# Performance work log

Measured on AMD Instinct MI355X. Metric: run time of the kernel, lower is better.

Reference implementation:

```python
import jax, jax.numpy as jnp
import numpy as np

N_NODES = 50000
N_EDGES = 320000
IN_FEAT = 128
HIDDEN = 256
N_CLASSES = 40
BN_EPS = 1e-5


def _gcn_norm(edge_index, n_nodes):
    # Add self-loops (PyG gcn_norm default) and compute sym-normalized weights
    loops = jnp.arange(n_nodes, dtype=edge_index.dtype)
    src = jnp.concatenate([edge_index[0], loops])
    dst = jnp.concatenate([edge_index[1], loops])
    ones = jnp.ones(src.shape[0], dtype=jnp.float32)
    deg = jax.ops.segment_sum(ones, dst, num_segments=n_nodes)
    dinv = jnp.where(deg > 0, jax.lax.rsqrt(deg), 0.0)
    norm = dinv[src] * dinv[dst]  # [E+N]
    return src, dst, norm


def _gcn_conv(x, src, dst, norm, W, b, n_nodes):
    xw = x @ W                                   # [N, F_out]
    msg = norm[:, None] * xw[src]                # [E+N, F_out] gather
    out = jax.ops.segment_sum(msg, dst, num_segments=n_nodes)  # scatter-add
    return out + b


def _batchnorm(x, gamma, beta):
    mean = jnp.mean(x, axis=0)
    var = jnp.mean(jnp.square(x - mean), axis=0)  # biased, training-mode stats
    return (x - mean) * jax.lax.rsqrt(var + BN_EPS) * gamma + beta


def setup_inputs() -> dict:
    key = jax.random.key(0)
    ks = jax.random.split(key, 8)
    x = jax.random.normal(ks[0], (N_NODES, IN_FEAT), dtype=jnp.float32)
    edge_index = jax.random.randint(ks[1], (2, N_EDGES), 0, N_NODES, dtype=jnp.int64)
    s1 = 1.0 / np.sqrt(IN_FEAT)
    s2 = 1.0 / np.sqrt(HIDDEN)
    return {
        "x": x,
        "edge_index": edge_index,
        "W1": jax.random.normal(ks[2], (IN_FEAT, HIDDEN), dtype=jnp.float32) * s1,
        "b1": jnp.zeros((HIDDEN,), dtype=jnp.float32),
        "g1": jnp.ones((HIDDEN,), dtype=jnp.float32),
        "be1": jnp.zeros((HIDDEN,), dtype=jnp.float32),
        "W2": jax.random.normal(ks[3], (HIDDEN, HIDDEN), dtype=jnp.float32) * s2,
        "b2": jnp.zeros((HIDDEN,), dtype=jnp.float32),
        "g2": jnp.ones((HIDDEN,), dtype=jnp.float32),
        "be2": jnp.zeros((HIDDEN,), dtype=jnp.float32),
        "W3": jax.random.normal(ks[4], (HIDDEN, N_CLASSES), dtype=jnp.float32) * s2,
        "b3": jnp.zeros((N_CLASSES,), dtype=jnp.float32),
    }


def reference(x, edge_index, W1, b1, g1, be1, W2, b2, g2, be2, W3, b3):
    n = x.shape[0]
    src, dst, norm = _gcn_norm(edge_index, n)
    # layer 1
    h = _gcn_conv(x, src, dst, norm, W1, b1, n)
    h = jax.nn.relu(_batchnorm(h, g1, be1))
    # layer 2
    h = _gcn_conv(h, src, dst, norm, W2, b2, n)
    h = jax.nn.relu(_batchnorm(h, g2, be2))
    # output layer
    h = _gcn_conv(h, src, dst, norm, W3, b3, n)
    return jax.nn.log_softmax(h, axis=1)
```

## Files before the change

### kernel.cpp

```cpp
#include <hip/hip_runtime.h>

#define N_NODES 50000
#define N_EDGES 320000
#define IN_FEAT 128
#define HIDDEN  256
#define NCLS    40
#define BN_EPS  1e-5f

#define SCAN_B  256
#define SCAN_NB ((N_NODES + SCAN_B - 1) / SCAN_B)
#define GNB     (N_NODES / 16)

#define PREP_HIST_NB  (N_EDGES / 256)
#define PREP_CVT_NB   (N_NODES * IN_FEAT / 8 / 256)
#define PREP_PACK_NB  54
#define BNA_NB        (N_NODES * HIDDEN / 8 / 256)

typedef __attribute__((ext_vector_type(8))) _Float16 f16x8;
typedef __attribute__((ext_vector_type(2))) _Float16 f16x2;
typedef __attribute__((ext_vector_type(4))) float f32x4;

__device__ __forceinline__ f16x2 pkmax0(f16x2 a) {
    return __builtin_elementwise_max(a, (f16x2)(_Float16)0.f);
}

__device__ __forceinline__ void packB_unit(const float* __restrict__ W,
                                           _Float16* __restrict__ Bp,
                                           int nt, int kt, int nkt, int M, int lane) {
    const int n = nt * 16 + (lane & 15);
    const int kb = kt * 32 + (lane >> 4) * 8;
    _Float16* dst = Bp + (((size_t)nt * nkt + kt) * 64 + lane) * 8;
#pragma unroll
    for (int j = 0; j < 8; j++)
        dst[j] = (n < M) ? (_Float16)W[(size_t)(kb + j) * M + n] : (_Float16)0.f;
}

__global__ __launch_bounds__(256) void k_prep(const int* __restrict__ e_dst,
                                              int* __restrict__ counts,
                                              const float* __restrict__ x,
                                              _Float16* __restrict__ Xh,
                                              const float* __restrict__ W1,
                                              const float* __restrict__ W2,
                                              const float* __restrict__ W3,
                                              _Float16* __restrict__ W1p,
                                              _Float16* __restrict__ W2p,
                                              _Float16* __restrict__ W3p) {
    const int b = blockIdx.x;
    const int tid = threadIdx.x;
    if (b < PREP_HIST_NB) {
        const int e = b * 256 + tid;
        atomicAdd(&counts[e_dst[e]], 1);
    } else if (b < PREP_HIST_NB + PREP_CVT_NB) {
        const int i = (b - PREP_HIST_NB) * 256 + tid;
        float4 a = *(const float4*)(x + (size_t)i * 8);
        float4 c = *(const float4*)(x + (size_t)i * 8 + 4);
        f16x8 o = {(_Float16)a.x, (_Float16)a.y, (_Float16)a.z, (_Float16)a.w,
                   (_Float16)c.x, (_Float16)c.y, (_Float16)c.z, (_Float16)c.w};
        *(f16x8*)&Xh[(size_t)i * 8] = o;
    } else {
        const int wave = tid >> 6, lane = tid & 63;
        const int u = (b - PREP_HIST_NB - PREP_CVT_NB) * 4 + wave;
        if (u < 64) {
            packB_unit(W1, W1p, u >> 2, u & 3, 4, HIDDEN, lane);
        } else if (u < 192) {
            const int v = u - 64;
            packB_unit(W2, W2p, v >> 3, v & 7, 8, HIDDEN, lane);
        } else {
            const int v = u - 192;
            packB_unit(W3, W3p, v >> 3, v & 7, 8, NCLS, lane);
        }
    }
}

__global__ __launch_bounds__(SCAN_B) void k_scan_local(const int* __restrict__ counts,
                                                       int* __restrict__ rowp,
                                                       int* __restrict__ partials) {
    __shared__ int s[SCAN_B];
    const int tid = threadIdx.x;
    const int i = blockIdx.x * SCAN_B + tid;
    int v = (i < N_NODES) ? counts[i] : 0;
    s[tid] = v;
    __syncthreads();
    for (int off = 1; off < SCAN_B; off <<= 1) {
        int t = (tid >= off) ? s[tid - off] : 0;
        __syncthreads();
        s[tid] += t;
        __syncthreads();
    }
    if (i < N_NODES) rowp[i] = s[tid] - v;
    if (tid == SCAN_B - 1) partials[blockIdx.x] = s[SCAN_B - 1];
}

__global__ __launch_bounds__(SCAN_B) void k_scan_add(int* __restrict__ rowp,
                                                     int* __restrict__ cursor,
                                                     const int* __restrict__ partials,
                                                     const int* __restrict__ counts,
                                                     float* __restrict__ dinv) {
    __shared__ int s[SCAN_B];
    const int tid = threadIdx.x;
    const int b = blockIdx.x;
    int v = (tid < b) ? partials[tid] : 0;
    s[tid] = v;
    __syncthreads();
    for (int off = SCAN_B / 2; off > 0; off >>= 1) {
        if (tid < off) s[tid] += s[tid + off];
        __syncthreads();
    }
    const int offset = s[0];
    const int i = b * SCAN_B + tid;
    if (i < N_NODES) {
        int r = rowp[i] + offset;
        rowp[i] = r;
        cursor[i] = r;
        dinv[i] = rsqrtf(1.0f + (float)counts[i]);
    }
    if (b == 0 && tid == 0) rowp[N_NODES] = N_EDGES;
}

__global__ void k_scatter(const int* __restrict__ src, const int* __restrict__ dst,
                          int* __restrict__ cursor, const float* __restrict__ dinv,
                          int2* __restrict__ edat) {
    int e = blockIdx.x * blockDim.x + threadIdx.x;
    if (e < N_EDGES) {
        int d = dst[e], s = src[e];
        int p = atomicAdd(&cursor[d], 1);
        int2 v; v.x = s; v.y = __float_as_int(dinv[s] * dinv[d]);
        edat[p] = v;
    }
}

template <int KIN>
__global__ __launch_bounds__(256, 4) void k_fused(const _Float16* __restrict__ Xin,
                                                  const int* __restrict__ rowp,
                                                  const int2* __restrict__ edat,
                                                  const float* __restrict__ dinv,
                                                  const _Float16* __restrict__ Bp,
                                                  const float* __restrict__ bias,
                                                  _Float16* __restrict__ C,
                                                  float* __restrict__ bnp2) {
    constexpr int nkt = KIN / 32;
    constexpr int LROW = KIN + 8;
    constexpr int RW8 = KIN / 8;
    constexpr int NL = KIN / 128;
    __shared__ __align__(16) _Float16 At[16 * LROW];
    const int wave = threadIdx.x >> 6;
    const int lane = threadIdx.x & 63;
    const int sub  = lane >> 4;
    const int t    = lane & 15;
    const int sb   = lane & 48;
    const int node = blockIdx.x * 16 + wave * 4 + sub;

    const int e0 = rowp[node];
    const int deg = rowp[node + 1] - e0;
    int   pidx = 0;
    float pw   = 0.f;
    if (t < deg) {
        const int2 e = edat[e0 + t];
        pidx = e.x;
        pw = __int_as_float(e.y);
    }
    const float dd = dinv[node];
    const f16x2 sw2 = (f16x2)(_Float16)(dd * dd);

    const f16x8* __restrict__ Xr = (const f16x8*)Xin;
    union U8 { f16x8 v; f16x2 h[4]; };

    U8 a[NL];
#pragma unroll
    for (int q = 0; q < NL; q++) {
        U8 r; r.v = Xr[(size_t)node * RW8 + q * 16 + t];
#pragma unroll
        for (int p = 0; p < 4; p++) a[q].h[p] = sw2 * r.h[p];
    }

    auto fmaacc = [&](U8& r, _Float16 w, int q) {
        const f16x2 w2 = (f16x2)w;
#pragma unroll
        for (int p = 0; p < 4; p++) a[q].h[p] = w2 * r.h[p] + a[q].h[p];
    };

    if constexpr (NL == 1) {
        int bi[16]; _Float16 bw[16];
#pragma unroll
        for (int j = 0; j < 16; j++) {
            const int   v  = __shfl(pidx, sb + j);
            const float wv = __shfl(pw,  sb + j);
            const bool ok = j < deg;
            bi[j] = ok ? v : node;
            bw[j] = ok ? (_Float16)wv : (_Float16)0.f;
        }
        U8 r0, r1, r2, r3, r4, r5, r6, r7, r8, r9, r10, r11, r12, r13, r14, r15;
        r0.v  = Xr[(size_t)bi[0]  * RW8 + t];
        r1.v  = Xr[(size_t)bi[1]  * RW8 + t];
        r2.v  = Xr[(size_t)bi[2]  * RW8 + t];
        r3.v  = Xr[(size_t)bi[3]  * RW8 + t];
        r4.v  = Xr[(size_t)bi[4]  * RW8 + t];
        r5.v  = Xr[(size_t)bi[5]  * RW8 + t];
        r6.v  = Xr[(size_t)bi[6]  * RW8 + t];
        r7.v  = Xr[(size_t)bi[7]  * RW8 + t];
        r8.v  = Xr[(size_t)bi[8]  * RW8 + t];
        r9.v  = Xr[(size_t)bi[9]  * RW8 + t];
        r10.v = Xr[(size_t)bi[10] * RW8 + t];
        r11.v = Xr[(size_t)bi[11] * RW8 + t];
        r12.v = Xr[(size_t)bi[12] * RW8 + t];
        r13.v = Xr[(size_t)bi[13] * RW8 + t];
        r14.v = Xr[(size_t)bi[14] * RW8 + t];
        r15.v = Xr[(size_t)bi[15] * RW8 + t];
        asm volatile("" : "+v"(r0.v), "+v"(r1.v), "+v"(r2.v), "+v"(r3.v),
                          "+v"(r4.v), "+v"(r5.v), "+v"(r6.v), "+v"(r7.v),
                          "+v"(r8.v), "+v"(r9.v), "+v"(r10.v), "+v"(r11.v),
                          "+v"(r12.v), "+v"(r13.v), "+v"(r14.v), "+v"(r15.v));
        fmaacc(r0, bw[0], 0);   fmaacc(r1, bw[1], 0);
        fmaacc(r2, bw[2], 0);   fmaacc(r3, bw[3], 0);
        fmaacc(r4, bw[4], 0);   fmaacc(r5, bw[5], 0);
        fmaacc(r6, bw[6], 0);   fmaacc(r7, bw[7], 0);
        fmaacc(r8, bw[8], 0);   fmaacc(r9, bw[9], 0);
        fmaacc(r10, bw[10], 0); fmaacc(r11, bw[11], 0);
        fmaacc(r12, bw[12], 0); fmaacc(r13, bw[13], 0);
        fmaacc(r14, bw[14], 0); fmaacc(r15, bw[15], 0);
    } else {
        auto batch8 = [&](int j0) {
            int bi[8]; _Float16 bw[8];
#pragma unroll
            for (int j = 0; j < 8; j++) {
                const int   v  = __shfl(pidx, sb + j0 + j);
                const float wv = __shfl(pw,  sb + j0 + j);
                const bool ok = (j0 + j) < deg;
                bi[j] = ok ? v : node;
                bw[j] = ok ? (_Float16)wv : (_Float16)0.f;
            }
            U8 r0, r1, r2, r3, r4, r5, r6, r7;
            U8 s0, s1, s2, s3, s4, s5, s6, s7;
            r0.v = Xr[(size_t)bi[0] * RW8 + t];
            s0.v = Xr[(size_t)bi[0] * RW8 + 16 + t];
            r1.v = Xr[(size_t)bi[1] * RW8 + t];
            s1.v = Xr[(size_t)bi[1] * RW8 + 16 + t];
            r2.v = Xr[(size_t)bi[2] * RW8 + t];
            s2.v = Xr[(size_t)bi[2] * RW8 + 16 + t];
            r3.v = Xr[(size_t)bi[3] * RW8 + t];
            s3.v = Xr[(size_t)bi[3] * RW8 + 16 + t];
            r4.v = Xr[(size_t)bi[4] * RW8 + t];
            s4.v = Xr[(size_t)bi[4] * RW8 + 16 + t];
            r5.v = Xr[(size_t)bi[5] * RW8 + t];
            s5.v = Xr[(size_t)bi[5] * RW8 + 16 + t];
            r6.v = Xr[(size_t)bi[6] * RW8 + t];
            s6.v = Xr[(size_t)bi[6] * RW8 + 16 + t];
            r7.v = Xr[(size_t)bi[7] * RW8 + t];
            s7.v = Xr[(size_t)bi[7] * RW8 + 16 + t];
            asm volatile("" : "+v"(r0.v), "+v"(r1.v), "+v"(r2.v), "+v"(r3.v),
                              "+v"(r4.v), "+v"(r5.v), "+v"(r6.v), "+v"(r7.v),
                              "+v"(s0.v), "+v"(s1.v), "+v"(s2.v), "+v"(s3.v),
                              "+v"(s4.v), "+v"(s5.v), "+v"(s6.v), "+v"(s7.v));
            fmaacc(r0, bw[0], 0); fmaacc(s0, bw[0], 1);
            fmaacc(r1, bw[1], 0); fmaacc(s1, bw[1], 1);
            fmaacc(r2, bw[2], 0); fmaacc(s2, bw[2], 1);
            fmaacc(r3, bw[3], 0); fmaacc(s3, bw[3], 1);
            fmaacc(r4, bw[4], 0); fmaacc(s4, bw[4], 1);
            fmaacc(r5, bw[5], 0); fmaacc(s5, bw[5], 1);
            fmaacc(r6, bw[6], 0); fmaacc(s6, bw[6], 1);
            fmaacc(r7, bw[7], 0); fmaacc(s7, bw[7], 1);
        };
        batch8(0);
        if (__any(deg > 8)) batch8(8);
    }
    if (__any(deg > 16)) {
        for (int j = 16; j < deg; j++) {
            const int2 ed = edat[e0 + j];
            const f16x2 w2 = (f16x2)(_Float16)__int_as_float(ed.y);
#pragma unroll
            for (int q = 0; q < NL; q++) {
                U8 r; r.v = Xr[(size_t)ed.x * RW8 + q * 16 + t];
#pragma unroll
                for (int p = 0; p < 4; p++) a[q].h[p] = w2 * r.h[p] + a[q].h[p];
            }
        }
    }
#pragma unroll
    for (int q = 0; q < NL; q++)
        *(f16x8*)&At[(wave * 4 + sub) * LROW + q * 128 + t * 8] = a[q].v;
    __syncthreads();

    const int rowb = blockIdx.x * 16;
    const int ntile0 = wave * 4;
    const _Float16* aL = &At[(lane & 15) * LROW + (lane >> 4) * 8];
    f32x4 acc[4] = {};
#pragma unroll
    for (int kt = 0; kt < nkt; kt++) {
        f16x8 af = *(const f16x8*)(aL + kt * 32);
#pragma unroll
        for (int nt = 0; nt < 4; nt++) {
            f16x8 bfr = *(const f16x8*)(Bp + (((size_t)(ntile0 + nt) * nkt + kt) * 64 + lane) * 8);
            acc[nt] = __builtin_amdgcn_mfma_f32_16x16x32_f16(af, bfr, acc[nt], 0, 0, 0);
        }
    }
    const int rg = lane >> 4, cc = lane & 15;
    float s[4], q2[4];
#pragma unroll
    for (int nt = 0; nt < 4; nt++) {
        const int col = (ntile0 + nt) * 16 + cc;
        const float b = bias[col];
        f32x4 a2 = acc[nt];
        a2[0] += b; a2[1] += b; a2[2] += b; a2[3] += b;
        const size_t base = (size_t)(rowb + rg * 4) * HIDDEN + col;
#pragma unroll
        for (int i = 0; i < 4; i++) C[base + (size_t)i * HIDDEN] = (_Float16)a2[i];
        s[nt] = a2[0] + a2[1] + a2[2] + a2[3];
        q2[nt] = a2[0]*a2[0] + a2[1]*a2[1] + a2[2]*a2[2] + a2[3]*a2[3];
    }
#pragma unroll
    for (int nt = 0; nt < 4; nt++) {
        s[nt] += __shfl_xor(s[nt], 16); s[nt] += __shfl_xor(s[nt], 32);
        q2[nt] += __shfl_xor(q2[nt], 16); q2[nt] += __shfl_xor(q2[nt], 32);
    }
    if (lane < 16) {
        float* dst = bnp2 + ((blockIdx.x & 31) * 512) + ntile0 * 16 + lane;
#pragma unroll
        for (int nt = 0; nt < 4; nt++) {
            atomicAdd(&dst[nt * 16], s[nt]);
            atomicAdd(&dst[nt * 16 + 256], q2[nt]);
        }
    }
}

__global__ __launch_bounds__(256) void k_bnprep(const float* __restrict__ bnp2,
                                                const float* __restrict__ g,
                                                const float* __restrict__ be,
                                                float* __restrict__ scale,
                                                float* __restrict__ shift) {
    const int f = threadIdx.x;
    float s = 0.f, q = 0.f;
#pragma unroll
    for (int b = 0; b < 32; b++) {
        s += bnp2[(size_t)b * 512 + f];
        q += bnp2[(size_t)b * 512 + 256 + f];
    }
    const float inv_n = 1.0f / (float)N_NODES;
    float mean = s * inv_n;
    float var = q * inv_n - mean * mean;
    var = fmaxf(var, 0.f);
    float sc = g[f] * rsqrtf(var + BN_EPS);
    scale[f] = sc;
    shift[f] = be[f] - mean * sc;
}

__global__ __launch_bounds__(256) void k_bnapply(_Float16* __restrict__ H,
                                                 const float* __restrict__ scale,
                                                 const float* __restrict__ shift) {
    const size_t i = (size_t)blockIdx.x * 256 + threadIdx.x;
    const int f0 = (int)(i & 31) * 8;
    union U8 { f16x8 v; f16x2 h[4]; } r;
    r.v = ((const f16x8*)H)[i];
#pragma unroll
    for (int p = 0; p < 4; p++) {
        f16x2 sc = {(_Float16)scale[f0 + 2 * p], (_Float16)scale[f0 + 2 * p + 1]};
        f16x2 sh = {(_Float16)shift[f0 + 2 * p], (_Float16)shift[f0 + 2 * p + 1]};
        r.h[p] = pkmax0(sc * r.h[p] + sh);
    }
    ((f16x8*)H)[i] = r.v;
}

template <int K_>
__global__ __launch_bounds__(64) void k_gemm3(const _Float16* __restrict__ A,
                                              const _Float16* __restrict__ Bp,
                                              const float* __restrict__ scale,
                                              const float* __restrict__ shift,
                                              _Float16* __restrict__ C) {
    constexpr int nkt = K_ / 32;
    constexpr int MT = 3;
    const int lane = threadIdx.x & 63;
    const int rowb = blockIdx.x * 16;
    const int koff = (lane >> 4) * 8;
    const _Float16* aptr = A + (size_t)(rowb + (lane & 15)) * K_ + koff;
    f32x4 acc[MT] = {};
#pragma unroll
    for (int kt = 0; kt < nkt; kt++) {
        union { f16x8 v; f16x2 h[4]; } au, tu;
        au.v = *(const f16x8*)(aptr + kt * 32);
        const int kb = kt * 32 + koff;
#pragma unroll
        for (int p = 0; p < 4; p++) {
            f16x2 sc2 = {(_Float16)scale[kb + 2 * p], (_Float16)scale[kb + 2 * p + 1]};
            f16x2 sh2 = {(_Float16)shift[kb + 2 * p], (_Float16)shift[kb + 2 * p + 1]};
            tu.h[p] = pkmax0(sc2 * au.h[p] + sh2);
        }
#pragma unroll
        for (int nt = 0; nt < MT; nt++) {
            f16x8 bfr = *(const f16x8*)(Bp + (((size_t)nt * nkt + kt) * 64 + lane) * 8);
            acc[nt] = __builtin_amdgcn_mfma_f32_16x16x32_f16(tu.v, bfr, acc[nt], 0, 0, 0);
        }
    }
    const int rg = lane >> 4, cc = lane & 15;
#pragma unroll
    for (int nt = 0; nt < MT; nt++) {
        const int col = nt * 16 + cc;
        if (col < NCLS) {
            const size_t base = (size_t)(rowb + rg * 4) * NCLS + col;
#pragma unroll
            for (int i = 0; i < 4; i++) C[base + (size_t)i * NCLS] = (_Float16)acc[nt][i];
        }
    }
}

__global__ __launch_bounds__(256) void k_out(const _Float16* __restrict__ XW,
                                             const int* __restrict__ rowp,
                                             const int2* __restrict__ edat,
                                             const float* __restrict__ dinv,
                                             const float* __restrict__ bias,
                                             float* __restrict__ out) {
    const int wave = threadIdx.x >> 6;
    const int lane = threadIdx.x & 63;
    const int node = blockIdx.x * 4 + wave;
    const float dd = dinv[node];
    const bool act = lane < NCLS;
    const int e0 = rowp[node];
    const int deg = rowp[node + 1] - e0;
    int pidx = 0; float pw = 0.f;
    if (lane < deg) {
        const int2 e = edat[e0 + lane];
        pidx = e.x; pw = __int_as_float(e.y);
    }
    const _Float16* Xl = XW + lane;
    float acc = 0.f;
    if (act) acc = dd * dd * (float)Xl[(size_t)node * NCLS];
    auto batch8 = [&](int j0) {
        int bi[8]; float bw[8];
#pragma unroll
        for (int j = 0; j < 8; j++) {
            const int   v  = __shfl(pidx, j0 + j);
            const float wv = __shfl(pw,  j0 + j);
            const bool ok = (j0 + j) < deg;
            bi[j] = ok ? v : node;
            bw[j] = ok ? wv : 0.f;
        }
        if (act) {
            _Float16 v0 = Xl[(size_t)bi[0] * NCLS];
            _Float16 v1 = Xl[(size_t)bi[1] * NCLS];
            _Float16 v2 = Xl[(size_t)bi[2] * NCLS];
            _Float16 v3 = Xl[(size_t)bi[3] * NCLS];
            _Float16 v4 = Xl[(size_t)bi[4] * NCLS];
            _Float16 v5 = Xl[(size_t)bi[5] * NCLS];
            _Float16 v6 = Xl[(size_t)bi[6] * NCLS];
            _Float16 v7 = Xl[(size_t)bi[7] * NCLS];
            asm volatile("" : "+v"(v0), "+v"(v1), "+v"(v2), "+v"(v3),
                              "+v"(v4), "+v"(v5), "+v"(v6), "+v"(v7));
            acc += bw[0] * (float)v0 + bw[1] * (float)v1
                 + bw[2] * (float)v2 + bw[3] * (float)v3
                 + bw[4] * (float)v4 + bw[5] * (float)v5
                 + bw[6] * (float)v6 + bw[7] * (float)v7;
        }
    };
    batch8(0);
    if (deg > 8) {
        batch8(8);
        if (deg > 16) {
            batch8(16);
            if (deg > 24) {
                batch8(24);
                if (deg > 32) {
                    for (int j = 32; j < deg; j++) {
                        const int2 ed = edat[e0 + j];
                        if (act) acc += __int_as_float(ed.y) * (float)Xl[(size_t)ed.x * NCLS];
                    }
                }
            }
        }
    }
    if (act) acc += bias[lane];
    float m = act ? acc : -1e30f;
#pragma unroll
    for (int off = 32; off > 0; off >>= 1) m = fmaxf(m, __shfl_xor(m, off));
    float e = act ? expf(acc - m) : 0.f;
#pragma unroll
    for (int off = 32; off > 0; off >>= 1) e += __shfl_xor(e, off);
    const float lse = m + logf(e);
    if (act) out[node * NCLS + lane] = acc - lse;
}

extern "C" void kernel_launch(void* const* d_in, const int* in_sizes, int n_in,
                              void* d_out, int out_size, void* d_ws, size_t ws_size,
                              hipStream_t stream) {
    const float* x   = (const float*)d_in[0];
    const int*   ei  = (const int*)d_in[1];
    const float* W1  = (const float*)d_in[2];
    const float* b1  = (const float*)d_in[3];
    const float* g1  = (const float*)d_in[4];
    const float* be1 = (const float*)d_in[5];
    const float* W2  = (const float*)d_in[6];
    const float* b2  = (const float*)d_in[7];
    const float* g2  = (const float*)d_in[8];
    const float* be2 = (const float*)d_in[9];
    const float* W3  = (const float*)d_in[10];
    const float* b3  = (const float*)d_in[11];
    float* out = (float*)d_out;

    const int* e_src = ei;
    const int* e_dst = ei + N_EDGES;

    char* w = (char*)d_ws;
    _Float16* Xh  = (_Float16*)w;              w += (size_t)N_NODES * IN_FEAT * 2;
    _Float16* H1h = (_Float16*)w;              w += (size_t)N_NODES * HIDDEN * 2;
    _Float16* H2h = (_Float16*)w;              w += (size_t)N_NODES * HIDDEN * 2;
    _Float16* XW3h = (_Float16*)w;             w += (size_t)N_NODES * NCLS * 2;
    float* dinv   = (float*)w;                 w += (size_t)N_NODES * 4;
    int2*  edat   = (int2*)w;                  w += (size_t)N_EDGES * 8;
    int*   counts = (int*)w;                   w += (size_t)N_NODES * 4;
    float* bnp2a  = (float*)w;                 w += (size_t)32 * 512 * 4;
    float* bnp2b  = (float*)w;                 w += (size_t)32 * 512 * 4;
    int*   rowp   = (int*)w;                   w += (size_t)(N_NODES + 4) * 4;
    int*   cursor = (int*)w;                   w += (size_t)N_NODES * 4;
    int*   partials=(int*)w;                   w += 256 * 4;
    float* scale1 = (float*)w;                 w += 256 * 4;
    float* shift1 = (float*)w;                 w += 256 * 4;
    float* scale2 = (float*)w;                 w += 256 * 4;
    float* shift2 = (float*)w;                 w += 256 * 4;
    _Float16* W1p = (_Float16*)w;              w += (size_t)16 * 4 * 64 * 8 * 2;
    _Float16* W2p = (_Float16*)w;              w += (size_t)16 * 8 * 64 * 8 * 2;
    _Float16* W3p = (_Float16*)w;              w += (size_t)3 * 8 * 64 * 8 * 2;

    const int EB = (N_EDGES + 255) / 256;

    hipMemsetAsync(counts, 0, (size_t)N_NODES * 4 + 2 * (size_t)32 * 512 * 4, stream);
    k_prep<<<PREP_HIST_NB + PREP_CVT_NB + PREP_PACK_NB, 256, 0, stream>>>(
        e_dst, counts, x, Xh, W1, W2, W3, W1p, W2p, W3p);
    k_scan_local<<<SCAN_NB, SCAN_B, 0, stream>>>(counts, rowp, partials);
    k_scan_add<<<SCAN_NB, SCAN_B, 0, stream>>>(rowp, cursor, partials, counts, dinv);
    k_scatter<<<EB, 256, 0, stream>>>(e_src, e_dst, cursor, dinv, edat);

    k_fused<IN_FEAT><<<GNB, 256, 0, stream>>>(
        Xh, rowp, edat, dinv, W1p, b1, H1h, bnp2a);
    k_bnprep<<<1, 256, 0, stream>>>(bnp2a, g1, be1, scale1, shift1);
    k_bnapply<<<BNA_NB, 256, 0, stream>>>(H1h, scale1, shift1);

    k_fused<HIDDEN><<<GNB, 256, 0, stream>>>(
        H1h, rowp, edat, dinv, W2p, b2, H2h, bnp2b);
    k_bnprep<<<1, 256, 0, stream>>>(bnp2b, g2, be2, scale2, shift2);

    k_gemm3<HIDDEN><<<GNB, 64, 0, stream>>>(H2h, W3p, scale2, shift2, XW3h);
    k_out<<<N_NODES / 4, 256, 0, stream>>>(XW3h, rowp, edat, dinv, b3, out);
}
```

Before: 245.7 us.

## Fuse layer-1 BatchNorm+ReLU into layer-2 gather and pad XW3 rows to 64

Removes the separate BN-apply pass over H1 and instead applies scale/shift/ReLU to every gathered neighbor row inside the layer-2 aggregation kernel. This saves one read and one write of the 50000x256 fp16 activation, at the cost of redoing the BN math once per edge rather than once per node and holding extra registers for the per-lane scale/shift. It also pads the output-layer XW3 buffer row stride from 40 to 64 halves, which aligns the rows for the final gather.

```diff
diff --git a/kernel.cpp b/kernel.cpp
--- a/kernel.cpp
+++ b/kernel.cpp
@@ -5,6 +5,7 @@
 #define IN_FEAT 128
 #define HIDDEN  256
 #define NCLS    40
+#define OPAD    64
 #define BN_EPS  1e-5f
 
 #define SCAN_B  256
@@ -14,7 +15,6 @@
 #define PREP_HIST_NB  (N_EDGES / 256)
 #define PREP_CVT_NB   (N_NODES * IN_FEAT / 8 / 256)
 #define PREP_PACK_NB  54
-#define BNA_NB        (N_NODES * HIDDEN / 8 / 256)
 
 typedef __attribute__((ext_vector_type(8))) _Float16 f16x8;
 typedef __attribute__((ext_vector_type(2))) _Float16 f16x2;
@@ -129,11 +129,13 @@
     }
 }
 
-template <int KIN>
+template <int KIN, bool BN>
 __global__ __launch_bounds__(256, 4) void k_fused(const _Float16* __restrict__ Xin,
                                                   const int* __restrict__ rowp,
                                                   const int2* __restrict__ edat,
                                                   const float* __restrict__ dinv,
+                                                  const float* __restrict__ scale,
+                                                  const float* __restrict__ shift,
                                                   const _Float16* __restrict__ Bp,
                                                   const float* __restrict__ bias,
                                                   _Float16* __restrict__ C,
@@ -162,6 +164,18 @@
     const float dd = dinv[node];
     const f16x2 sw2 = (f16x2)(_Float16)(dd * dd);
 
+    f16x2 scq[NL][4], shq[NL][4];
+    if constexpr (BN) {
+#pragma unroll
+        for (int q = 0; q < NL; q++)
+#pragma unroll
+            for (int p = 0; p < 4; p++) {
+                const int f0 = q * 128 + t * 8 + 2 * p;
+                scq[q][p] = f16x2{(_Float16)scale[f0], (_Float16)scale[f0 + 1]};
+                shq[q][p] = f16x2{(_Float16)shift[f0], (_Float16)shift[f0 + 1]};
+            }
+    }
+
     const f16x8* __restrict__ Xr = (const f16x8*)Xin;
     union U8 { f16x8 v; f16x2 h[4]; };
 
@@ -170,13 +184,21 @@
     for (int q = 0; q < NL; q++) {
         U8 r; r.v = Xr[(size_t)node * RW8 + q * 16 + t];
 #pragma unroll
-        for (int p = 0; p < 4; p++) a[q].h[p] = sw2 * r.h[p];
-    }
-
-    auto fmaacc = [&](U8& r, _Float16 w, int q) {
+        for (int p = 0; p < 4; p++) {
+            f16x2 v = r.h[p];
+            if constexpr (BN) v = pkmax0(scq[q][p] * v + shq[q][p]);
+            a[q].h[p] = sw2 * v;
+        }
+    }
+
+    auto proc = [&](U8& r, _Float16 w, int q) {
         const f16x2 w2 = (f16x2)w;
 #pragma unroll
-        for (int p = 0; p < 4; p++) a[q].h[p] = w2 * r.h[p] + a[q].h[p];
+        for (int p = 0; p < 4; p++) {
+            f16x2 v = r.h[p];
+            if constexpr (BN) v = pkmax0(scq[q][p] * v + shq[q][p]);
+            a[q].h[p] = w2 * v + a[q].h[p];
+        }
     };
 
     if constexpr (NL == 1) {
@@ -210,14 +232,14 @@
                           "+v"(r4.v), "+v"(r5.v), "+v"(r6.v), "+v"(r7.v),
                           "+v"(r8.v), "+v"(r9.v), "+v"(r10.v), "+v"(r11.v),
                           "+v"(r12.v), "+v"(r13.v), "+v"(r14.v), "+v"(r15.v));
-        fmaacc(r0, bw[0], 0);   fmaacc(r1, bw[1], 0);
-        fmaacc(r2, bw[2], 0);   fmaacc(r3, bw[3], 0);
-        fmaacc(r4, bw[4], 0);   fmaacc(r5, bw[5], 0);
-        fmaacc(r6, bw[6], 0);   fmaacc(r7, bw[7], 0);
-        fmaacc(r8, bw[8], 0);   fmaacc(r9, bw[9], 0);
-        fmaacc(r10, bw[10], 0); fmaacc(r11, bw[11], 0);
-        fmaacc(r12, bw[12], 0); fmaacc(r13, bw[13], 0);
-        fmaacc(r14, bw[14], 0); fmaacc(r15, bw[15], 0);
+        proc(r0, bw[0], 0);   proc(r1, bw[1], 0);
+        proc(r2, bw[2], 0);   proc(r3, bw[3], 0);
+        proc(r4, bw[4], 0);   proc(r5, bw[5], 0);
+        proc(r6, bw[6], 0);   proc(r7, bw[7], 0);
+        proc(r8, bw[8], 0);   proc(r9, bw[9], 0);
+        proc(r10, bw[10], 0); proc(r11, bw[11], 0);
+        proc(r12, bw[12], 0); proc(r13, bw[13], 0);
+        proc(r14, bw[14], 0); proc(r15, bw[15], 0);
     } else {
         auto batch8 = [&](int j0) {
             int bi[8]; _Float16 bw[8];
@@ -251,14 +273,14 @@
                               "+v"(r4.v), "+v"(r5.v), "+v"(r6.v), "+v"(r7.v),
                               "+v"(s0.v), "+v"(s1.v), "+v"(s2.v), "+v"(s3.v),
                               "+v"(s4.v), "+v"(s5.v), "+v"(s6.v), "+v"(s7.v));
-            fmaacc(r0, bw[0], 0); fmaacc(s0, bw[0], 1);
-            fmaacc(r1, bw[1], 0); fmaacc(s1, bw[1], 1);
-            fmaacc(r2, bw[2], 0); fmaacc(s2, bw[2], 1);
-            fmaacc(r3, bw[3], 0); fmaacc(s3, bw[3], 1);
-            fmaacc(r4, bw[4], 0); fmaacc(s4, bw[4], 1);
-            fmaacc(r5, bw[5], 0); fmaacc(s5, bw[5], 1);
-            fmaacc(r6, bw[6], 0); fmaacc(s6, bw[6], 1);
-            fmaacc(r7, bw[7], 0); fmaacc(s7, bw[7], 1);
+            proc(r0, bw[0], 0); proc(s0, bw[0], 1);
+            proc(r1, bw[1], 0); proc(s1, bw[1], 1);
+            proc(r2, bw[2], 0); proc(s2, bw[2], 1);
+            proc(r3, bw[3], 0); proc(s3, bw[3], 1);
+            proc(r4, bw[4], 0); proc(s4, bw[4], 1);
+            proc(r5, bw[5], 0); proc(s5, bw[5], 1);
+            proc(r6, bw[6], 0); proc(s6, bw[6], 1);
+            proc(r7, bw[7], 0); proc(s7, bw[7], 1);
         };
         batch8(0);
         if (__any(deg > 8)) batch8(8);
@@ -266,12 +288,11 @@
     if (__any(deg > 16)) {
         for (int j = 16; j < deg; j++) {
             const int2 ed = edat[e0 + j];
-            const f16x2 w2 = (f16x2)(_Float16)__int_as_float(ed.y);
+            const _Float16 wj = (_Float16)__int_as_float(ed.y);
 #pragma unroll
             for (int q = 0; q < NL; q++) {
                 U8 r; r.v = Xr[(size_t)ed.x * RW8 + q * 16 + t];
-#pragma unroll
-                for (int p = 0; p < 4; p++) a[q].h[p] = w2 * r.h[p] + a[q].h[p];
+                proc(r, wj, q);
             }
         }
     }
@@ -341,22 +362,6 @@
     float sc = g[f] * rsqrtf(var + BN_EPS);
     scale[f] = sc;
     shift[f] = be[f] - mean * sc;
-}
-
-__global__ __launch_bounds__(256) void k_bnapply(_Float16* __restrict__ H,
-                                                 const float* __restrict__ scale,
-                                                 const float* __restrict__ shift) {
-    const size_t i = (size_t)blockIdx.x * 256 + threadIdx.x;
-    const int f0 = (int)(i & 31) * 8;
-    union U8 { f16x8 v; f16x2 h[4]; } r;
-    r.v = ((const f16x8*)H)[i];
-#pragma unroll
-    for (int p = 0; p < 4; p++) {
-        f16x2 sc = {(_Float16)scale[f0 + 2 * p], (_Float16)scale[f0 + 2 * p + 1]};
-        f16x2 sh = {(_Float16)shift[f0 + 2 * p], (_Float16)shift[f0 + 2 * p + 1]};
-        r.h[p] = pkmax0(sc * r.h[p] + sh);
-    }
-    ((f16x8*)H)[i] = r.v;
 }
 
 template <int K_>
@@ -394,9 +399,9 @@
     for (int nt = 0; nt < MT; nt++) {
         const int col = nt * 16 + cc;
         if (col < NCLS) {
-            const size_t base = (size_t)(rowb + rg * 4) * NCLS + col;
-#pragma unroll
-            for (int i = 0; i < 4; i++) C[base + (size_t)i * NCLS] = (_Float16)acc[nt][i];
+            const size_t base = (size_t)(rowb + rg * 4) * OPAD + col;
+#pragma unroll
+            for (int i = 0; i < 4; i++) C[base + (size_t)i * OPAD] = (_Float16)acc[nt][i];
         }
     }
 }
@@ -421,7 +426,7 @@
     }
     const _Float16* Xl = XW + lane;
     float acc = 0.f;
-    if (act) acc = dd * dd * (float)Xl[(size_t)node * NCLS];
+    if (act) acc = dd * dd * (float)Xl[(size_t)node * OPAD];
     auto batch8 = [&](int j0) {
         int bi[8]; float bw[8];
 #pragma unroll
@@ -433,14 +438,14 @@
             bw[j] = ok ? wv : 0.f;
         }
         if (act) {
-            _Float16 v0 = Xl[(size_t)bi[0] * NCLS];
-            _Float16 v1 = Xl[(size_t)bi[1] * NCLS];
-            _Float16 v2 = Xl[(size_t)bi[2] * NCLS];
-            _Float16 v3 = Xl[(size_t)bi[3] * NCLS];
-            _Float16 v4 = Xl[(size_t)bi[4] * NCLS];
-            _Float16 v5 = Xl[(size_t)bi[5] * NCLS];
-            _Float16 v6 = Xl[(size_t)bi[6] * NCLS];
-            _Float16 v7 = Xl[(size_t)bi[7] * NCLS];
+            _Float16 v0 = Xl[(size_t)bi[0] * OPAD];
+            _Float16 v1 = Xl[(size_t)bi[1] * OPAD];
+            _Float16 v2 = Xl[(size_t)bi[2] * OPAD];
+            _Float16 v3 = Xl[(size_t)bi[3] * OPAD];
+            _Float16 v4 = Xl[(size_t)bi[4] * OPAD];
+            _Float16 v5 = Xl[(size_t)bi[5] * OPAD];
+            _Float16 v6 = Xl[(size_t)bi[6] * OPAD];
+            _Float16 v7 = Xl[(size_t)bi[7] * OPAD];
             asm volatile("" : "+v"(v0), "+v"(v1), "+v"(v2), "+v"(v3),
                               "+v"(v4), "+v"(v5), "+v"(v6), "+v"(v7));
             acc += bw[0] * (float)v0 + bw[1] * (float)v1
@@ -459,7 +464,7 @@
                 if (deg > 32) {
                     for (int j = 32; j < deg; j++) {
                         const int2 ed = edat[e0 + j];
-                        if (act) acc += __int_as_float(ed.y) * (float)Xl[(size_t)ed.x * NCLS];
+                        if (act) acc += __int_as_float(ed.y) * (float)Xl[(size_t)ed.x * OPAD];
                     }
                 }
             }
@@ -500,7 +505,7 @@
     _Float16* Xh  = (_Float16*)w;              w += (size_t)N_NODES * IN_FEAT * 2;
     _Float16* H1h = (_Float16*)w;              w += (size_t)N_NODES * HIDDEN * 2;
     _Float16* H2h = (_Float16*)w;              w += (size_t)N_NODES * HIDDEN * 2;
-    _Float16* XW3h = (_Float16*)w;             w += (size_t)N_NODES * NCLS * 2;
+    _Float16* XW3h = (_Float16*)w;             w += (size_t)N_NODES * OPAD * 2;
     float* dinv   = (float*)w;                 w += (size_t)N_NODES * 4;
     int2*  edat   = (int2*)w;                  w += (size_t)N_EDGES * 8;
     int*   counts = (int*)w;                   w += (size_t)N_NODES * 4;
@@ -526,13 +531,12 @@
     k_scan_add<<<SCAN_NB, SCAN_B, 0, stream>>>(rowp, cursor, partials, counts, dinv);
     k_scatter<<<EB, 256, 0, stream>>>(e_src, e_dst, cursor, dinv, edat);
 
-    k_fused<IN_FEAT><<<GNB, 256, 0, stream>>>(
-        Xh, rowp, edat, dinv, W1p, b1, H1h, bnp2a);
+    k_fused<IN_FEAT, false><<<GNB, 256, 0, stream>>>(
+        Xh, rowp, edat, dinv, nullptr, nullptr, W1p, b1, H1h, bnp2a);
     k_bnprep<<<1, 256, 0, stream>>>(bnp2a, g1, be1, scale1, shift1);
-    k_bnapply<<<BNA_NB, 256, 0, stream>>>(H1h, scale1, shift1);
-
-    k_fused<HIDDEN><<<GNB, 256, 0, stream>>>(
-        H1h, rowp, edat, dinv, W2p, b2, H2h, bnp2b);
+
+    k_fused<HIDDEN, true><<<GNB, 256, 0, stream>>>(
+        H1h, rowp, edat, dinv, scale1, shift1, W2p, b2, H2h, bnp2b);
     k_bnprep<<<1, 256, 0, stream>>>(bnp2b, g2, be2, scale2, shift2);
 
     k_gemm3<HIDDEN><<<GNB, 64, 0, stream>>>(H2h, W3p, scale2, shift2, XW3h);
```

New measurement: 242.7 us. Within noise of the previous version (-1.2%).
